# Kernel tuning notes

Measured on AMD Instinct MI355X. Metric: run time of the kernel, lower is better.

The kernel has to match this reference:

```python
import jax, jax.numpy as jnp
import numpy as np

N, TO, TI, H = 8, 2048, 2048, 128
MASK_FILL = -99999.0  # module uses -99999.0, not -inf


def setup_inputs() -> dict:
    key = jax.random.key(0)
    kq, kv, km = jax.random.split(key, 3)
    queries = jax.random.normal(kq, (N, TO, H), dtype=jnp.float32)
    values = jax.random.normal(kv, (N, TI, H), dtype=jnp.float32)
    # mask is applied to scores.view(-1, Ti) -> shape (N*To, Ti), True = masked
    mask = jax.random.randint(km, (N * TO, TI), 0, 2).astype(bool)
    return {"queries": queries, "values": values, "mask": mask}


def reference(queries, values, mask):
    n, to, h = queries.shape
    ti = values.shape[1]
    # N x To x Ti scores (no 1/sqrt(H) scaling in the original)
    scores = jnp.einsum("nth,nsh->nts", queries, values)
    scores = jnp.where(mask.reshape(n, to, ti), MASK_FILL, scores)
    attention_distribution = jax.nn.softmax(scores, axis=-1)
    attention_output = jnp.einsum("nts,nsh->nth", attention_distribution, values)
    return attention_output, attention_distribution
```

## Files before the change

kernel.cpp:

```cpp
#include <hip/hip_runtime.h>

#define NB  8
#define TOQ 2048
#define TIV 2048
#define HD  128

typedef float f32x4 __attribute__((ext_vector_type(4)));
typedef short s16x8 __attribute__((ext_vector_type(8)));
typedef unsigned short ushort4v __attribute__((ext_vector_type(4)));
typedef unsigned short ushort8v __attribute__((ext_vector_type(8)));

__device__ __forceinline__ unsigned short f2bf(float f) {
    unsigned u = __float_as_uint(f);
    return (unsigned short)((u + 0x7FFFu + ((u >> 16) & 1u)) >> 16);
}
__device__ __forceinline__ float bf2f(unsigned short h) {
    return __uint_as_float(((unsigned)h) << 16);
}

__device__ __forceinline__ void split8(const float4 a, const float4 b,
                                       ushort8v& h, ushort8v& l) {
    const float x[8] = {a.x, a.y, a.z, a.w, b.x, b.y, b.z, b.w};
    #pragma unroll
    for (int j = 0; j < 8; ++j) {
        const unsigned short hi = f2bf(x[j]);
        h[j] = hi;
        l[j] = f2bf(x[j] - bf2f(hi));
    }
}

__device__ __forceinline__ void gload16(const void* g, void* l) {
    __builtin_amdgcn_global_load_lds(
        (const __attribute__((address_space(1))) void*)g,
        (__attribute__((address_space(3))) void*)l, 16, 0, 0);
}

__global__ __launch_bounds__(256) void k0_split(
    const float* __restrict__ Q, const float* __restrict__ V,
    unsigned short* __restrict__ Qh, unsigned short* __restrict__ Ql,
    unsigned short* __restrict__ Vh, unsigned short* __restrict__ Vl)
{
    const size_t i = ((size_t)blockIdx.x * 256 + threadIdx.x) * 8;
    const float* src = blockIdx.y ? V : Q;
    unsigned short* dh = blockIdx.y ? Vh : Qh;
    unsigned short* dl = blockIdx.y ? Vl : Ql;
    const float4 a = *(const float4*)&src[i];
    const float4 b = *(const float4*)&src[i + 4];
    ushort8v h, l;
    split8(a, b, h, l);
    *(ushort8v*)&dh[i] = h;
    *(ushort8v*)&dl[i] = l;
}

__global__ __launch_bounds__(256) void k0_vt(
    const float* __restrict__ V, unsigned short* __restrict__ VT)
{
    __shared__ unsigned short tile[64][68];
    const int n  = blockIdx.z;
    const int s0 = blockIdx.x * 64;
    const int h0 = blockIdx.y * 64;
    const int t  = threadIdx.x;

    #pragma unroll
    for (int it = 0; it < 4; ++it) {
        const int f = t + it * 256;
        const int r = f >> 4;
        const int c = f & 15;
        const float4 v = *(const float4*)&V[((size_t)(n * TIV + s0 + r)) * HD + h0 + 4 * c];
        tile[4 * c + 0][r] = f2bf(v.x);
        tile[4 * c + 1][r] = f2bf(v.y);
        tile[4 * c + 2][r] = f2bf(v.z);
        tile[4 * c + 3][r] = f2bf(v.w);
    }
    __syncthreads();

    #pragma unroll
    for (int it = 0; it < 2; ++it) {
        const int f  = t + it * 256;
        const int hh = f >> 3;
        const int sc = f & 7;
        ushort8v o;
        #pragma unroll
        for (int j = 0; j < 8; ++j) o[j] = tile[hh][8 * sc + j];
        *(ushort8v*)&VT[((size_t)(n * HD + h0 + hh)) * TIV + s0 + 8 * sc] = o;
    }
}

__global__ __launch_bounds__(512) void k1_w8(
    const unsigned short* __restrict__ QhG, const unsigned short* __restrict__ QlG,
    const unsigned short* __restrict__ VhG, const unsigned short* __restrict__ VlG,
    const int* __restrict__ M, unsigned short* __restrict__ Eb,
    float* __restrict__ part)
{
    __shared__ unsigned short qh_l[128 * 32], ql_l[128 * 32];
    __shared__ unsigned short vh_l[128 * 32], vl_l[128 * 32];

    const int n    = blockIdx.z;
    const int tt   = blockIdx.y * 128;
    const int ts   = blockIdx.x * 128;
    const int t    = threadIdx.x;
    const int lane = t & 63;
    const int wave = t >> 6;
    const int wr   = wave >> 2;
    const int wc   = wave & 3;
    const int lr   = lane & 15;
    const int kg   = lane >> 4;

    f32x4 acc[4][2];
    #pragma unroll
    for (int i = 0; i < 4; ++i)
        #pragma unroll
        for (int j = 0; j < 2; ++j) acc[i][j] = (f32x4)0.f;

    for (int h0 = 0; h0 < HD; h0 += 32) {
        {
            const int c   = wave * 64 + lane;
            const int row = c >> 2;
            const int kb  = (c & 3) * 8;
            const int lb  = wave * 512;
            const size_t qo = ((size_t)(n * TOQ + tt + row)) * HD + h0 + kb;
            const size_t vo = ((size_t)(n * TIV + ts + row)) * HD + h0 + kb;
            gload16(QhG + qo, qh_l + lb);
            gload16(QlG + qo, ql_l + lb);
            gload16(VhG + vo, vh_l + lb);
            gload16(VlG + vo, vl_l + lb);
        }
        __syncthreads();

        s16x8 aH[4], aL[4];
        #pragma unroll
        for (int fm = 0; fm < 4; ++fm) {
            const int off = (wr * 64 + fm * 16 + lr) * 32 + kg * 8;
            aH[fm] = *(const s16x8*)(vh_l + off);
            aL[fm] = *(const s16x8*)(vl_l + off);
        }
        #pragma unroll
        for (int fn = 0; fn < 2; ++fn) {
            const int off = (wc * 32 + fn * 16 + lr) * 32 + kg * 8;
            const s16x8 bH = *(const s16x8*)(qh_l + off);
            const s16x8 bL = *(const s16x8*)(ql_l + off);
            #pragma unroll
            for (int fm = 0; fm < 4; ++fm) {
                acc[fm][fn] = __builtin_amdgcn_mfma_f32_16x16x32_bf16(aH[fm], bH, acc[fm][fn], 0, 0, 0);
                acc[fm][fn] = __builtin_amdgcn_mfma_f32_16x16x32_bf16(aH[fm], bL, acc[fm][fn], 0, 0, 0);
                acc[fm][fn] = __builtin_amdgcn_mfma_f32_16x16x32_bf16(aL[fm], bH, acc[fm][fn], 0, 0, 0);
            }
        }
        __syncthreads();
    }

    #pragma unroll
    for (int fn = 0; fn < 2; ++fn) {
        const int to_g = tt + wc * 32 + fn * 16 + lr;
        const size_t rowbase = ((size_t)n * TOQ + to_g) * TIV;
        float rs = 0.f;
        #pragma unroll
        for (int fm = 0; fm < 4; ++fm) {
            const int ti_g = ts + wr * 64 + fm * 16 + kg * 4;
            const int4 mv = *(const int4*)&M[rowbase + ti_g];
            float4 e;
            e.x = mv.x ? 0.f : __expf(acc[fm][fn][0]);
            e.y = mv.y ? 0.f : __expf(acc[fm][fn][1]);
            e.z = mv.z ? 0.f : __expf(acc[fm][fn][2]);
            e.w = mv.w ? 0.f : __expf(acc[fm][fn][3]);
            ushort4v eb;
            eb[0] = f2bf(e.x); eb[1] = f2bf(e.y);
            eb[2] = f2bf(e.z); eb[3] = f2bf(e.w);
            *(ushort4v*)&Eb[rowbase + ti_g] = eb;
            rs += (e.x + e.y) + (e.z + e.w);
        }
        rs += __shfl_xor(rs, 16, 64);
        rs += __shfl_xor(rs, 32, 64);
        if (kg == 0)
            part[((size_t)n * TOQ + to_g) * 32 + blockIdx.x * 2 + wr] = rs;
    }
}

__global__ __launch_bounds__(256) void k1_reg(
    const float* __restrict__ Q, const float* __restrict__ V,
    const int* __restrict__ M, float* __restrict__ E,
    float* __restrict__ part)
{
    __shared__ unsigned short qhi[128 * 32], qlo[128 * 32];
    __shared__ unsigned short vhi[128 * 32], vlo[128 * 32];

    const int n    = blockIdx.z;
    const int tt   = blockIdx.y * 128;
    const int ts   = blockIdx.x * 128;
    const int t    = threadIdx.x;
    const int lane = t & 63;
    const int wave = t >> 6;
    const int wr   = wave >> 1;
    const int wc   = wave & 1;
    const int lr   = lane & 15;
    const int kg   = lane >> 4;

    const float* Qb = Q + ((size_t)n * TOQ + tt) * HD;
    const float* Vb = V + ((size_t)n * TIV + ts) * HD;

    f32x4 acc[4][4];
    #pragma unroll
    for (int i = 0; i < 4; ++i)
        #pragma unroll
        for (int j = 0; j < 4; ++j) acc[i][j] = (f32x4)0.f;

    for (int h0 = 0; h0 < HD; h0 += 32) {
        #pragma unroll
        for (int it = 0; it < 2; ++it) {
            const int i   = t + it * 256;
            const int row = i >> 2;
            const int kb  = i & 3;
            const float* qs = Qb + (size_t)row * HD + h0 + kb * 8;
            const float* vs = Vb + (size_t)row * HD + h0 + kb * 8;
            const float4 q0 = *(const float4*)qs, q1 = *(const float4*)(qs + 4);
            const float4 v0 = *(const float4*)vs, v1 = *(const float4*)(vs + 4);
            ushort8v qh, ql, vh, vl;
            split8(q0, q1, qh, ql);
            split8(v0, v1, vh, vl);
            *(ushort8v*)(qhi + i * 8) = qh;
            *(ushort8v*)(qlo + i * 8) = ql;
            *(ushort8v*)(vhi + i * 8) = vh;
            *(ushort8v*)(vlo + i * 8) = vl;
        }
        __syncthreads();

        s16x8 aH[4], aL[4];
        #pragma unroll
        for (int fm = 0; fm < 4; ++fm) {
            const int off = (wr * 64 + fm * 16 + lr) * 32 + kg * 8;
            aH[fm] = *(const s16x8*)(vhi + off);
            aL[fm] = *(const s16x8*)(vlo + off);
        }
        #pragma unroll
        for (int fn = 0; fn < 4; ++fn) {
            const int off = (wc * 64 + fn * 16 + lr) * 32 + kg * 8;
            const s16x8 bH = *(const s16x8*)(qhi + off);
            const s16x8 bL = *(const s16x8*)(qlo + off);
            #pragma unroll
            for (int fm = 0; fm < 4; ++fm) {
                acc[fm][fn] = __builtin_amdgcn_mfma_f32_16x16x32_bf16(aH[fm], bH, acc[fm][fn], 0, 0, 0);
                acc[fm][fn] = __builtin_amdgcn_mfma_f32_16x16x32_bf16(aH[fm], bL, acc[fm][fn], 0, 0, 0);
                acc[fm][fn] = __builtin_amdgcn_mfma_f32_16x16x32_bf16(aL[fm], bH, acc[fm][fn], 0, 0, 0);
            }
        }
        __syncthreads();
    }

    #pragma unroll
    for (int fn = 0; fn < 4; ++fn) {
        const int to_g = tt + wc * 64 + fn * 16 + lr;
        const size_t rowbase = ((size_t)n * TOQ + to_g) * TIV;
        float rs = 0.f;
        #pragma unroll
        for (int fm = 0; fm < 4; ++fm) {
            const int ti_g = ts + wr * 64 + fm * 16 + kg * 4;
            const int4 mv = *(const int4*)&M[rowbase + ti_g];
            float4 e;
            e.x = mv.x ? 0.f : __expf(acc[fm][fn][0]);
            e.y = mv.y ? 0.f : __expf(acc[fm][fn][1]);
            e.z = mv.z ? 0.f : __expf(acc[fm][fn][2]);
            e.w = mv.w ? 0.f : __expf(acc[fm][fn][3]);
            *(float4*)&E[rowbase + ti_g] = e;
            rs += (e.x + e.y) + (e.z + e.w);
        }
        rs += __shfl_xor(rs, 16, 64);
        rs += __shfl_xor(rs, 32, 64);
        if (kg == 0)
            part[((size_t)n * TOQ + to_g) * 32 + blockIdx.x * 2 + wr] = rs;
    }
}

__global__ __launch_bounds__(256) void k2_rowsum(
    const float* __restrict__ part, float* __restrict__ rec)
{
    const int row = blockIdx.x * 256 + threadIdx.x;
    const float4* p4 = (const float4*)(part + (size_t)row * 32);
    float s = 0.f;
    #pragma unroll
    for (int i = 0; i < 8; ++i) {
        const float4 v = p4[i];
        s += (v.x + v.y) + (v.z + v.w);
    }
    rec[row] = 1.f / s;
}

__global__ __launch_bounds__(512) void k3_occ(
    const unsigned short* __restrict__ Eb, const unsigned short* __restrict__ VT,
    const float* __restrict__ rec, float* __restrict__ P, float* __restrict__ O)
{
    __shared__ float red[4][16][132];

    const int n    = blockIdx.y;
    const int r0   = blockIdx.x * 16;
    const int t    = threadIdx.x;
    const int q    = t >> 6;
    const int lane = t & 63;
    const int lr   = lane & 15;
    const int kg   = lane >> 4;

    const int rowg = r0 + lr;
    const float rc = rec[n * TOQ + rowg];
    const unsigned short* Erow = Eb + ((size_t)n * TOQ + rowg) * TIV;
    float* Prow = P + ((size_t)n * TOQ + rowg) * TIV;
    const unsigned short* VTb = VT + (size_t)n * HD * TIV;

    f32x4 acc[8];
    #pragma unroll
    for (int fn = 0; fn < 8; ++fn) acc[fn] = (f32x4)0.f;

    const int kbase = q * 256 + kg * 8;

    #pragma unroll 2
    for (int k0 = 0; k0 < 256; k0 += 32) {
        const int k = kbase + k0;
        const ushort8v ev = *(const ushort8v*)&Erow[k];
        float pv[8];
        #pragma unroll
        for (int j = 0; j < 8; ++j) pv[j] = bf2f(ev[j]) * rc;

        float4 p0, p1;
        p0.x = pv[0]; p0.y = pv[1]; p0.z = pv[2]; p0.w = pv[3];
        p1.x = pv[4]; p1.y = pv[5]; p1.z = pv[6]; p1.w = pv[7];
        *(float4*)&Prow[k]     = p0;
        *(float4*)&Prow[k + 4] = p1;

        s16x8 a;
        #pragma unroll
        for (int j = 0; j < 8; ++j) a[j] = (short)f2bf(pv[j]);

        #pragma unroll
        for (int fn = 0; fn < 8; ++fn) {
            const s16x8 b = *(const s16x8*)&VTb[(size_t)(fn * 16 + lr) * TIV + k];
            acc[fn] = __builtin_amdgcn_mfma_f32_16x16x32_bf16(a, b, acc[fn], 0, 0, 0);
        }
    }

    #define PARK(slot)                                                         \
        _Pragma("unroll") for (int fn = 0; fn < 8; ++fn)                       \
        _Pragma("unroll") for (int ri = 0; ri < 4; ++ri)                       \
            red[slot][kg * 4 + ri][fn * 16 + lr] = acc[fn][ri];
    #define GATHER(slot)                                                       \
        _Pragma("unroll") for (int fn = 0; fn < 8; ++fn)                       \
        _Pragma("unroll") for (int ri = 0; ri < 4; ++ri)                       \
            acc[fn][ri] += red[slot][kg * 4 + ri][fn * 16 + lr];

    if (q & 1) { PARK(q >> 1) }
    __syncthreads();
    if (!(q & 1)) { GATHER(q >> 1) }
    __syncthreads();
    if (!(q & 1) && (q & 2)) { PARK(q >> 2) }
    __syncthreads();
    if (!(q & 3)) { GATHER(q >> 2) }
    __syncthreads();
    if (q == 4) { PARK(0) }
    __syncthreads();
    if (q == 0) {
        GATHER(0)
        #pragma unroll
        for (int fn = 0; fn < 8; ++fn) {
            #pragma unroll
            for (int ri = 0; ri < 4; ++ri) {
                const int orow = r0 + kg * 4 + ri;
                O[((size_t)n * TOQ + orow) * HD + fn * 16 + lr] = acc[fn][ri];
            }
        }
    }
    #undef PARK
    #undef GATHER
}

__global__ __launch_bounds__(512) void k3_pv_old(
    float* __restrict__ EP, const unsigned short* __restrict__ VT,
    const float* __restrict__ rec, float* __restrict__ O)
{
    __shared__ float red[2][3][16][132];

    const int n    = blockIdx.y;
    const int r0   = blockIdx.x * 32;
    const int t    = threadIdx.x;
    const int wave = t >> 6;
    const int lane = t & 63;
    const int p    = wave >> 2;
    const int q    = wave & 3;
    const int lr   = lane & 15;
    const int kg   = lane >> 4;

    const int rowg = r0 + p * 16 + lr;
    const float rc = rec[n * TOQ + rowg];
    float* Erow = EP + ((size_t)n * TOQ + rowg) * TIV;
    const unsigned short* VTb = VT + (size_t)n * HD * TIV;

    f32x4 acc[8];
    #pragma unroll
    for (int fn = 0; fn < 8; ++fn) acc[fn] = (f32x4)0.f;

    const int kbase = q * 512 + kg * 8;

    #pragma unroll 2
    for (int k0 = 0; k0 < 512; k0 += 32) {
        const int k = kbase + k0;
        const float4 e0 = *(const float4*)&Erow[k];
        const float4 e1 = *(const float4*)&Erow[k + 4];
        float4 p0, p1;
        p0.x = e0.x * rc; p0.y = e0.y * rc; p0.z = e0.z * rc; p0.w = e0.w * rc;
        p1.x = e1.x * rc; p1.y = e1.y * rc; p1.z = e1.z * rc; p1.w = e1.w * rc;
        *(float4*)&Erow[k]     = p0;
        *(float4*)&Erow[k + 4] = p1;

        s16x8 a;
        a[0] = (short)f2bf(p0.x); a[1] = (short)f2bf(p0.y);
        a[2] = (short)f2bf(p0.z); a[3] = (short)f2bf(p0.w);
        a[4] = (short)f2bf(p1.x); a[5] = (short)f2bf(p1.y);
        a[6] = (short)f2bf(p1.z); a[7] = (short)f2bf(p1.w);

        #pragma unroll
        for (int fn = 0; fn < 8; ++fn) {
            const s16x8 b = *(const s16x8*)&VTb[(size_t)(fn * 16 + lr) * TIV + k];
            acc[fn] = __builtin_amdgcn_mfma_f32_16x16x32_bf16(a, b, acc[fn], 0, 0, 0);
        }
    }

    if (q != 0) {
        #pragma unroll
        for (int fn = 0; fn < 8; ++fn)
            #pragma unroll
            for (int ri = 0; ri < 4; ++ri)
                red[p][q - 1][kg * 4 + ri][fn * 16 + lr] = acc[fn][ri];
    }
    __syncthreads();
    if (q == 0) {
        #pragma unroll
        for (int fn = 0; fn < 8; ++fn) {
            #pragma unroll
            for (int ri = 0; ri < 4; ++ri) {
                const int orow = r0 + p * 16 + kg * 4 + ri;
                float o = acc[fn][ri];
                o += red[p][0][kg * 4 + ri][fn * 16 + lr];
                o += red[p][1][kg * 4 + ri][fn * 16 + lr];
                o += red[p][2][kg * 4 + ri][fn * 16 + lr];
                O[((size_t)n * TOQ + orow) * HD + fn * 16 + lr] = o;
            }
        }
    }
}

extern "C" void kernel_launch(void* const* d_in, const int* in_sizes, int n_in,
                              void* d_out, int out_size, void* d_ws, size_t ws_size,
                              hipStream_t stream)
{
    const float* Q = (const float*)d_in[0];
    const float* V = (const float*)d_in[1];
    const int*   M = (const int*)d_in[2];

    float* O = (float*)d_out;
    float* P = O + (size_t)NB * TOQ * HD;

    char* ws = (char*)d_ws;
    const size_t partB  = (size_t)NB * TOQ * 32 * 4;
    const size_t vtB    = (size_t)NB * HD * TIV * 2;
    const size_t elems  = (size_t)NB * TOQ * HD;
    const size_t sbytes = elems * 2;
    const size_t ebB    = (size_t)NB * TOQ * TIV * 2;

    float*          recb = (float*)ws;
    float*          part = (float*)(ws + (1 << 16));
    unsigned short* VT   = (unsigned short*)(ws + (1 << 16) + partB);
    const size_t splitOff = (1 << 16) + partB + vtB;
    const size_t ebOff    = splitOff + 4 * sbytes;
    const size_t need2    = ebOff + ebB;

    k0_vt<<<dim3(TIV / 64, HD / 64, NB), 256, 0, stream>>>(V, VT);

    if (ws_size >= need2) {
        unsigned short* Qh = (unsigned short*)(ws + splitOff);
        unsigned short* Ql = (unsigned short*)(ws + splitOff + sbytes);
        unsigned short* Vh = (unsigned short*)(ws + splitOff + 2 * sbytes);
        unsigned short* Vl = (unsigned short*)(ws + splitOff + 3 * sbytes);
        unsigned short* Eb = (unsigned short*)(ws + ebOff);
        k0_split<<<dim3((unsigned)(elems / 8 / 256), 2), 256, 0, stream>>>(Q, V, Qh, Ql, Vh, Vl);
        k1_w8   <<<dim3(TIV / 128, TOQ / 128, NB), 512, 0, stream>>>(Qh, Ql, Vh, Vl, M, Eb, part);
        k2_rowsum<<<dim3(NB * TOQ / 256), 256, 0, stream>>>(part, recb);
        k3_occ  <<<dim3(TOQ / 16, NB), 512, 0, stream>>>(Eb, VT, recb, P, O);
    } else {
        k1_reg  <<<dim3(TIV / 128, TOQ / 128, NB), 256, 0, stream>>>(Q, V, M, P, part);
        k2_rowsum<<<dim3(NB * TOQ / 256), 256, 0, stream>>>(part, recb);
        k3_pv_old<<<dim3(TOQ / 32, NB), 512, 0, stream>>>(P, VT, recb, O);
    }
}
```

Baseline: 176.2 us.

## Move probability write into rowsum kernel and defer normalization to output

The row-sum kernel now also normalizes the bf16 exponentials and writes the fp32 probability matrix, one wave per row. The PV kernel feeds the unnormalized bf16 exponentials straight into MFMA and scales the output rows by the reciprocal sum at the end. This takes the conversion and store work out of the MFMA loop. In exchange the bf16 E buffer is read twice, and rounding changes slightly because normalization now happens after accumulation.

```diff
diff --git a/kernel.cpp b/kernel.cpp
--- a/kernel.cpp
+++ b/kernel.cpp
@@ -270,6 +270,35 @@
     }
 }
 
+__global__ __launch_bounds__(256) void k2_norm(
+    const float* __restrict__ part, const unsigned short* __restrict__ Eb,
+    float* __restrict__ recb, float* __restrict__ P)
+{
+    const int row = blockIdx.x * 4 + (threadIdx.x >> 6);
+    const int l   = threadIdx.x & 63;
+
+    float s = part[(size_t)row * 32 + (l & 31)];
+    #pragma unroll
+    for (int off = 16; off > 0; off >>= 1) s += __shfl_xor(s, off, 32);
+    const float rc = 1.f / s;
+    if (l == 0) recb[row] = rc;
+
+    const unsigned short* Erow = Eb + (size_t)row * TIV;
+    float* Prow = P + (size_t)row * TIV;
+    #pragma unroll
+    for (int it = 0; it < 4; ++it) {
+        const int col = it * 512 + l * 8;
+        const ushort8v ev = *(const ushort8v*)&Erow[col];
+        float4 p0, p1;
+        p0.x = bf2f(ev[0]) * rc; p0.y = bf2f(ev[1]) * rc;
+        p0.z = bf2f(ev[2]) * rc; p0.w = bf2f(ev[3]) * rc;
+        p1.x = bf2f(ev[4]) * rc; p1.y = bf2f(ev[5]) * rc;
+        p1.z = bf2f(ev[6]) * rc; p1.w = bf2f(ev[7]) * rc;
+        *(float4*)&Prow[col]     = p0;
+        *(float4*)&Prow[col + 4] = p1;
+    }
+}
+
 __global__ __launch_bounds__(256) void k2_rowsum(
     const float* __restrict__ part, float* __restrict__ rec)
 {
@@ -284,9 +313,9 @@
     rec[row] = 1.f / s;
 }
 
-__global__ __launch_bounds__(512) void k3_occ(
+__global__ __launch_bounds__(512) void k3_o(
     const unsigned short* __restrict__ Eb, const unsigned short* __restrict__ VT,
-    const float* __restrict__ rec, float* __restrict__ P, float* __restrict__ O)
+    const float* __restrict__ recb, float* __restrict__ O)
 {
     __shared__ float red[4][16][132];
 
@@ -298,11 +327,8 @@
     const int lr   = lane & 15;
     const int kg   = lane >> 4;
 
-    const int rowg = r0 + lr;
-    const float rc = rec[n * TOQ + rowg];
-    const unsigned short* Erow = Eb + ((size_t)n * TOQ + rowg) * TIV;
-    float* Prow = P + ((size_t)n * TOQ + rowg) * TIV;
-    const unsigned short* VTb = VT + (size_t)n * HD * TIV;
+    const unsigned short* Erow = Eb + ((size_t)n * TOQ + r0 + lr) * TIV;
+    const unsigned short* VTb  = VT + (size_t)n * HD * TIV;
 
     f32x4 acc[8];
     #pragma unroll
@@ -313,21 +339,7 @@
     #pragma unroll 2
     for (int k0 = 0; k0 < 256; k0 += 32) {
         const int k = kbase + k0;
-        const ushort8v ev = *(const ushort8v*)&Erow[k];
-        float pv[8];
-        #pragma unroll
-        for (int j = 0; j < 8; ++j) pv[j] = bf2f(ev[j]) * rc;
-
-        float4 p0, p1;
-        p0.x = pv[0]; p0.y = pv[1]; p0.z = pv[2]; p0.w = pv[3];
-        p1.x = pv[4]; p1.y = pv[5]; p1.z = pv[6]; p1.w = pv[7];
-        *(float4*)&Prow[k]     = p0;
-        *(float4*)&Prow[k + 4] = p1;
-
-        s16x8 a;
-        #pragma unroll
-        for (int j = 0; j < 8; ++j) a[j] = (short)f2bf(pv[j]);
-
+        const s16x8 a = *(const s16x8*)&Erow[k];
         #pragma unroll
         for (int fn = 0; fn < 8; ++fn) {
             const s16x8 b = *(const s16x8*)&VTb[(size_t)(fn * 16 + lr) * TIV + k];
@@ -356,12 +368,16 @@
     __syncthreads();
     if (q == 0) {
         GATHER(0)
+        float rv[4];
+        #pragma unroll
+        for (int ri = 0; ri < 4; ++ri)
+            rv[ri] = recb[(size_t)n * TOQ + r0 + kg * 4 + ri];
         #pragma unroll
         for (int fn = 0; fn < 8; ++fn) {
             #pragma unroll
             for (int ri = 0; ri < 4; ++ri) {
                 const int orow = r0 + kg * 4 + ri;
-                O[((size_t)n * TOQ + orow) * HD + fn * 16 + lr] = acc[fn][ri];
+                O[((size_t)n * TOQ + orow) * HD + fn * 16 + lr] = acc[fn][ri] * rv[ri];
             }
         }
     }
@@ -479,8 +495,8 @@
         unsigned short* Eb = (unsigned short*)(ws + ebOff);
         k0_split<<<dim3((unsigned)(elems / 8 / 256), 2), 256, 0, stream>>>(Q, V, Qh, Ql, Vh, Vl);
         k1_w8   <<<dim3(TIV / 128, TOQ / 128, NB), 512, 0, stream>>>(Qh, Ql, Vh, Vl, M, Eb, part);
-        k2_rowsum<<<dim3(NB * TOQ / 256), 256, 0, stream>>>(part, recb);
-        k3_occ  <<<dim3(TOQ / 16, NB), 512, 0, stream>>>(Eb, VT, recb, P, O);
+        k2_norm <<<dim3(NB * TOQ / 4), 256, 0, stream>>>(part, Eb, recb, P);
+        k3_o    <<<dim3(TOQ / 16, NB), 512, 0, stream>>>(Eb, VT, recb, O);
     } else {
         k1_reg  <<<dim3(TIV / 128, TOQ / 128, NB), 256, 0, stream>>>(Q, V, M, P, part);
         k2_rowsum<<<dim3(NB * TOQ / 256), 256, 0, stream>>>(part, recb);
```

New measurement: 197.0 us. 1.12x slower.
